# Performance work log

Hardware: AMD Instinct MI355X
Metric: run time of the kernel (lower is better)

The kernel has to match this reference:

```python
import jax, jax.numpy as jnp
import numpy as np

N_NODES = 50000
N_EDGES = 1_600_000
D_IN = 128
D_HID = 128
N_CLASSES = 8
N_GRAPHS = 64


def setup_inputs() -> dict:
    key = jax.random.key(0)
    ks = jax.random.split(key, 8)
    x = jax.random.normal(ks[0], (N_NODES, D_IN), dtype=jnp.float32)
    edge_index = jax.random.randint(ks[1], (2, N_EDGES), 0, N_NODES, dtype=jnp.int32)
    graph_ids = jnp.sort(jax.random.randint(ks[2], (N_NODES,), 0, N_GRAPHS, dtype=jnp.int32))
    s = 1.0 / np.sqrt(D_HID)
    W1 = jax.random.normal(ks[3], (D_IN, D_HID), dtype=jnp.float32) * s
    b1 = jnp.zeros((D_HID,), dtype=jnp.float32)
    W2 = jax.random.normal(ks[4], (D_HID, D_HID), dtype=jnp.float32) * s
    b2 = jnp.zeros((D_HID,), dtype=jnp.float32)
    Wc = jax.random.normal(ks[5], (D_HID, N_CLASSES), dtype=jnp.float32) * s
    bc = jnp.zeros((N_CLASSES,), dtype=jnp.float32)
    return {"x": x, "edge_index": edge_index, "graph_ids": graph_ids,
            "W1": W1, "b1": b1, "W2": W2, "b2": b2, "Wc": Wc, "bc": bc}


def _gcn_layer(h, src, dst, norm, W, b):
    # message: gather source features, apply symmetric degree normalization
    msg = h[src] * norm[:, None]                       # [E, d]
    agg = jax.ops.segment_sum(msg, dst, num_segments=N_NODES)  # [N, d]
    return jax.nn.relu(agg @ W + b)


def reference(x, edge_index, graph_ids, W1, b1, W2, b2, Wc, bc):
    src, dst = edge_index[0], edge_index[1]
    ones_e = jnp.ones((N_EDGES,), dtype=x.dtype)
    deg = jax.ops.segment_sum(ones_e, dst, num_segments=N_NODES)
    deg_inv_sqrt = jnp.where(deg > 0, jax.lax.rsqrt(jnp.maximum(deg, 1.0)), 0.0)
    norm = deg_inv_sqrt[src] * deg_inv_sqrt[dst]       # [E]

    h = _gcn_layer(x, src, dst, norm, W1, b1)
    h = _gcn_layer(h, src, dst, norm, W2, b2)

    # per-graph mean pooling (segment mean over nodes of each graph)
    ones_n = jnp.ones((N_NODES,), dtype=h.dtype)
    counts = jax.ops.segment_sum(ones_n, graph_ids, num_segments=N_GRAPHS)
    pooled = jax.ops.segment_sum(h, graph_ids, num_segments=N_GRAPHS)
    pooled = pooled / jnp.maximum(counts, 1.0)[:, None]  # [G, d]

    logits = pooled @ Wc + bc                           # [G, n_classes]
    return logits
```

## Files before the change

### kernel.cpp

```cpp
#include <hip/hip_runtime.h>
#include <hip/hip_bf16.h>

#define D_HID 128
#define N_GRAPHS 64
#define N_CLASSES 8
#define NPB 16
#define CAP 96
#define KSWEEP 8

__device__ inline unsigned short f2b(float x) {
    unsigned int u = __float_as_uint(x);
    unsigned int r = (u + 0x7fffu + ((u >> 16) & 1u)) >> 16;
    return (unsigned short)r;
}
__device__ inline float b2f(unsigned short u) {
    return __uint_as_float((unsigned int)u << 16);
}

__global__ __launch_bounds__(256) void prep_kernel(const float* __restrict__ x,
                                                   unsigned int* __restrict__ xb,
                                                   int castBlocks, int n2,
                                                   const int* __restrict__ src,
                                                   const int* __restrict__ dst,
                                                   int* __restrict__ cursor,
                                                   unsigned short* __restrict__ csr16,
                                                   int E, int N, int fillBlocks, int rangeSize) {
    const int b = blockIdx.x;
    if (b < castBlocks) {
        int i = b * 256 + threadIdx.x;
        if (i < n2) {
            float a = x[2 * i], c = x[2 * i + 1];
            xb[i] = (unsigned int)f2b(a) | ((unsigned int)f2b(c) << 16);
        }
        return;
    }
    const int fb = b - castBlocks;
    const int sweep = fb / fillBlocks;
    const int blk = fb - sweep * fillBlocks;
    const int e = blk * 256 + threadIdx.x;
    if (e >= E) return;
    const int d = dst[e];
    const int lo = sweep * rangeSize;
    if (d < lo || d >= lo + rangeSize) return;
    const int s = src[e];
    int slot = atomicAdd(&cursor[d], 1);
    if (slot < CAP) csr16[(size_t)slot * N + d] = (unsigned short)s;
}

__global__ __launch_bounds__(256) void dis_counts_kernel(const int* __restrict__ deg,
                                                         float* __restrict__ dis,
                                                         const int* __restrict__ gid,
                                                         int* __restrict__ counts, int N) {
    int n = blockIdx.x * blockDim.x + threadIdx.x;
    if (n < N) {
        int v = deg[n];
        dis[n] = (v > 0) ? rsqrtf((float)v) : 0.0f;
    }
    if (blockIdx.x == 0 && threadIdx.x < N_GRAPHS) {
        int g = threadIdx.x;
        int lo0 = 0, hi0 = N;
        while (lo0 < hi0) { int mid = (lo0 + hi0) >> 1; if (gid[mid] < g) lo0 = mid + 1; else hi0 = mid; }
        int lo1 = lo0, hi1 = N;
        while (lo1 < hi1) { int mid = (lo1 + hi1) >> 1; if (gid[mid] < g + 1) lo1 = mid + 1; else hi1 = mid; }
        counts[g] = lo1 - lo0;
    }
}

__global__ __launch_bounds__(256) void layer_kernel(const unsigned short* __restrict__ h_in,
                                                    const int* __restrict__ deg,
                                                    const unsigned short* __restrict__ csr16,
                                                    const float* __restrict__ dis,
                                                    const float* __restrict__ W,
                                                    const float* __restrict__ bias,
                                                    unsigned short* __restrict__ h_out,
                                                    float* __restrict__ pooled,
                                                    const int* __restrict__ gid,
                                                    int fuse_pool, int N) {
    const int base = blockIdx.x * NPB;
    const int tid = threadIdx.x;
    const int wv = tid >> 6;
    const int lane = tid & 63;
    const int q = lane >> 4;
    const int ql = lane & 15;
    __shared__ float s_agg[NPB][D_HID];

    #pragma unroll
    for (int p = 0; p < 2; ++p) {
        const int n0 = base + wv * 4 + p * 2;
        const int n1 = n0 + 1;
        float acc0[8] = {0.f, 0.f, 0.f, 0.f, 0.f, 0.f, 0.f, 0.f};
        float acc1[8] = {0.f, 0.f, 0.f, 0.f, 0.f, 0.f, 0.f, 0.f};
        const int d0 = (n0 < N) ? min(deg[n0], CAP) : 0;
        const int d1 = (n1 < N) ? min(deg[n1], CAP) : 0;
        const int dm = max(d0, d1);
        for (int cb = 0; cb < dm; cb += 64) {
            const int cm = min(64, dm - cb);
            const int c0 = min(64, max(0, d0 - cb));
            const int c1 = min(64, max(0, d1 - cb));
            int idx0 = 0, idx1 = 0;
            float w0 = 0.0f, w1 = 0.0f;
            if (lane < c0) { idx0 = (int)csr16[(size_t)(cb + lane) * N + n0]; w0 = dis[idx0]; }
            if (lane < c1) { idx1 = (int)csr16[(size_t)(cb + lane) * N + n1]; w1 = dis[idx1]; }
            #pragma unroll 4
            for (int j = 0; j < cm; j += 4) {
                const int e = j + q;
                const int s0 = __shfl(idx0, e);
                const float ww0 = __shfl(w0, e);
                const int s1 = __shfl(idx1, e);
                const float ww1 = __shfl(w1, e);
                const uint4 r0 = *(const uint4*)&h_in[(size_t)s0 * D_HID + ql * 8];
                const uint4 r1 = *(const uint4*)&h_in[(size_t)s1 * D_HID + ql * 8];
                acc0[0] = fmaf(ww0, __uint_as_float(r0.x << 16), acc0[0]);
                acc0[1] = fmaf(ww0, __uint_as_float(r0.x & 0xffff0000u), acc0[1]);
                acc0[2] = fmaf(ww0, __uint_as_float(r0.y << 16), acc0[2]);
                acc0[3] = fmaf(ww0, __uint_as_float(r0.y & 0xffff0000u), acc0[3]);
                acc0[4] = fmaf(ww0, __uint_as_float(r0.z << 16), acc0[4]);
                acc0[5] = fmaf(ww0, __uint_as_float(r0.z & 0xffff0000u), acc0[5]);
                acc0[6] = fmaf(ww0, __uint_as_float(r0.w << 16), acc0[6]);
                acc0[7] = fmaf(ww0, __uint_as_float(r0.w & 0xffff0000u), acc0[7]);
                acc1[0] = fmaf(ww1, __uint_as_float(r1.x << 16), acc1[0]);
                acc1[1] = fmaf(ww1, __uint_as_float(r1.x & 0xffff0000u), acc1[1]);
                acc1[2] = fmaf(ww1, __uint_as_float(r1.y << 16), acc1[2]);
                acc1[3] = fmaf(ww1, __uint_as_float(r1.y & 0xffff0000u), acc1[3]);
                acc1[4] = fmaf(ww1, __uint_as_float(r1.z << 16), acc1[4]);
                acc1[5] = fmaf(ww1, __uint_as_float(r1.z & 0xffff0000u), acc1[5]);
                acc1[6] = fmaf(ww1, __uint_as_float(r1.w << 16), acc1[6]);
                acc1[7] = fmaf(ww1, __uint_as_float(r1.w & 0xffff0000u), acc1[7]);
            }
        }
        #pragma unroll
        for (int k = 0; k < 8; ++k) {
            acc0[k] += __shfl_down(acc0[k], 32);
            acc0[k] += __shfl_down(acc0[k], 16);
            acc1[k] += __shfl_down(acc1[k], 32);
            acc1[k] += __shfl_down(acc1[k], 16);
        }
        if (q == 0) {
            const float dn0 = (n0 < N) ? dis[n0] : 0.0f;
            const float dn1 = (n1 < N) ? dis[n1] : 0.0f;
            #pragma unroll
            for (int k = 0; k < 8; ++k) {
                s_agg[wv * 4 + p * 2 + 0][ql * 8 + k] = acc0[k] * dn0;
                s_agg[wv * 4 + p * 2 + 1][ql * 8 + k] = acc1[k] * dn1;
            }
        }
    }
    __syncthreads();

    const int t = tid & 127;
    const int nb = tid >> 7;
    float outv[8];
    const float bt = bias[t];
    #pragma unroll
    for (int i = 0; i < 8; ++i) outv[i] = bt;

    for (int k = 0; k < D_HID; k += 4) {
        const float w0 = W[(k + 0) * D_HID + t];
        const float w1 = W[(k + 1) * D_HID + t];
        const float w2 = W[(k + 2) * D_HID + t];
        const float w3 = W[(k + 3) * D_HID + t];
        #pragma unroll
        for (int i = 0; i < 8; ++i) {
            float4 a = *(const float4*)&s_agg[nb * 8 + i][k];
            outv[i] = fmaf(a.x, w0, outv[i]);
            outv[i] = fmaf(a.y, w1, outv[i]);
            outv[i] = fmaf(a.z, w2, outv[i]);
            outv[i] = fmaf(a.w, w3, outv[i]);
        }
    }

    #pragma unroll
    for (int i = 0; i < 8; ++i) {
        const int n = base + nb * 8 + i;
        if (n >= N) break;
        float v = fmaxf(outv[i], 0.0f);
        if (fuse_pool) {
            atomicAdd(&pooled[gid[n] * D_HID + t], v);
        } else {
            h_out[(size_t)n * D_HID + t] = f2b(v);
        }
    }
}

__global__ __launch_bounds__(128) void pool_kernel(const unsigned short* __restrict__ h,
                                                   const int* __restrict__ gid,
                                                   float* __restrict__ pooled,
                                                   int N, int nodes_per_block) {
    const int t = threadIdx.x;
    const int start = blockIdx.x * nodes_per_block;
    if (start >= N) return;
    const int endn = min(start + nodes_per_block, N);
    int cur = gid[start];
    float sum = 0.0f;
    for (int n = start; n < endn; ++n) {
        int g = gid[n];
        if (g != cur) {
            atomicAdd(&pooled[cur * D_HID + t], sum);
            cur = g; sum = 0.0f;
        }
        sum += b2f(h[(size_t)n * D_HID + t]);
    }
    atomicAdd(&pooled[cur * D_HID + t], sum);
}

__global__ __launch_bounds__(512) void classify_kernel(const float* __restrict__ pooled,
                                                       const int* __restrict__ counts,
                                                       const float* __restrict__ Wc,
                                                       const float* __restrict__ bc,
                                                       float* __restrict__ out) {
    const int g = threadIdx.x >> 3;
    const int c = threadIdx.x & 7;
    float inv = 1.0f / fmaxf((float)counts[g], 1.0f);
    float acc = bc[c];
    #pragma unroll 8
    for (int k = 0; k < D_HID; ++k) {
        acc = fmaf(pooled[g * D_HID + k] * inv, Wc[k * N_CLASSES + c], acc);
    }
    out[g * N_CLASSES + c] = acc;
}

extern "C" void kernel_launch(void* const* d_in, const int* in_sizes, int n_in,
                              void* d_out, int out_size, void* d_ws, size_t ws_size,
                              hipStream_t stream) {
    const float* x   = (const float*)d_in[0];
    const int* edge  = (const int*)d_in[1];
    const int* gid   = (const int*)d_in[2];
    const float* W1  = (const float*)d_in[3];
    const float* b1  = (const float*)d_in[4];
    const float* W2  = (const float*)d_in[5];
    const float* b2  = (const float*)d_in[6];
    const float* Wc  = (const float*)d_in[7];
    const float* bc  = (const float*)d_in[8];
    float* out       = (float*)d_out;

    const int E = in_sizes[1] / 2;
    const int N = in_sizes[2];
    const int* src = edge;
    const int* dst = edge + E;

    char* p = (char*)d_ws;
    auto take = [&](size_t bytes) {
        char* r = p;
        p += (bytes + 255) & ~(size_t)255;
        return r;
    };
    int*   cursor  = (int*)take((size_t)N * 4);
    float* dis     = (float*)take((size_t)N * 4);
    float* pooled  = (float*)take((size_t)N_GRAPHS * D_HID * 4);
    int*   counts  = (int*)take((size_t)N_GRAPHS * 4);
    unsigned short* csr16 = (unsigned short*)take((size_t)N * CAP * 2);
    unsigned short* xb  = (unsigned short*)take((size_t)N * D_HID * 2);
    unsigned short* h1b = (unsigned short*)take((size_t)N * D_HID * 2);
    size_t used = (size_t)(p - (char*)d_ws);
    size_t h2_bytes = (size_t)N * D_HID * 2;
    const bool separate_pool = (used + h2_bytes <= ws_size);
    unsigned short* h2b = separate_pool ? (unsigned short*)take(h2_bytes) : nullptr;

    hipMemsetAsync(cursor, 0, (size_t)N * 4, stream);
    hipMemsetAsync(pooled, 0, (size_t)N_GRAPHS * D_HID * 4, stream);

    const int EB = 256;
    const int n2 = (N * D_HID) / 2;
    const int castBlocks = (n2 + EB - 1) / EB;
    const int fillBlocks = (E + EB - 1) / EB;
    const int rangeSize = (N + KSWEEP - 1) / KSWEEP;
    prep_kernel<<<castBlocks + KSWEEP * fillBlocks, EB, 0, stream>>>(
        x, (unsigned int*)xb, castBlocks, n2, src, dst, cursor, csr16, E, N, fillBlocks, rangeSize);
    dis_counts_kernel<<<(N + EB - 1) / EB, EB, 0, stream>>>(cursor, dis, gid, counts, N);

    const int LG = (N + NPB - 1) / NPB;
    layer_kernel<<<LG, 256, 0, stream>>>(xb, cursor, csr16, dis, W1, b1, h1b, pooled, gid, 0, N);

    if (separate_pool) {
        layer_kernel<<<LG, 256, 0, stream>>>(h1b, cursor, csr16, dis, W2, b2, h2b, pooled, gid, 0, N);
        const int NPBLK = 32;
        pool_kernel<<<(N + NPBLK - 1) / NPBLK, 128, 0, stream>>>(h2b, gid, pooled, N, NPBLK);
    } else {
        layer_kernel<<<LG, 256, 0, stream>>>(h1b, cursor, csr16, dis, W2, b2, nullptr, pooled, gid, 1, N);
    }

    classify_kernel<<<1, 512, 0, stream>>>(pooled, counts, Wc, bc, out);
}
```

Baseline: 376.3 us.

## Pack bf16 source norm with index in CSR, vectorize cast, always fuse pooling

```diff
diff --git a/kernel.cpp b/kernel.cpp
--- a/kernel.cpp
+++ b/kernel.cpp
@@ -18,19 +18,22 @@
 }
 
 __global__ __launch_bounds__(256) void prep_kernel(const float* __restrict__ x,
-                                                   unsigned int* __restrict__ xb,
-                                                   int castBlocks, int n2,
+                                                   uint2* __restrict__ xb4,
+                                                   int castBlocks, int n4,
                                                    const int* __restrict__ src,
                                                    const int* __restrict__ dst,
                                                    int* __restrict__ cursor,
-                                                   unsigned short* __restrict__ csr16,
+                                                   unsigned int* __restrict__ csr32,
                                                    int E, int N, int fillBlocks, int rangeSize) {
     const int b = blockIdx.x;
     if (b < castBlocks) {
         int i = b * 256 + threadIdx.x;
-        if (i < n2) {
-            float a = x[2 * i], c = x[2 * i + 1];
-            xb[i] = (unsigned int)f2b(a) | ((unsigned int)f2b(c) << 16);
+        if (i < n4) {
+            float4 v = ((const float4*)x)[i];
+            uint2 o;
+            o.x = (unsigned int)f2b(v.x) | ((unsigned int)f2b(v.y) << 16);
+            o.y = (unsigned int)f2b(v.z) | ((unsigned int)f2b(v.w) << 16);
+            xb4[i] = o;
         }
         return;
     }
@@ -44,7 +47,7 @@
     if (d < lo || d >= lo + rangeSize) return;
     const int s = src[e];
     int slot = atomicAdd(&cursor[d], 1);
-    if (slot < CAP) csr16[(size_t)slot * N + d] = (unsigned short)s;
+    if (slot < CAP) csr32[(size_t)slot * N + d] = (unsigned int)s;
 }
 
 __global__ __launch_bounds__(256) void dis_counts_kernel(const int* __restrict__ deg,
@@ -66,16 +69,29 @@
     }
 }
 
-__global__ __launch_bounds__(256) void layer_kernel(const unsigned short* __restrict__ h_in,
-                                                    const int* __restrict__ deg,
-                                                    const unsigned short* __restrict__ csr16,
-                                                    const float* __restrict__ dis,
-                                                    const float* __restrict__ W,
-                                                    const float* __restrict__ bias,
-                                                    unsigned short* __restrict__ h_out,
-                                                    float* __restrict__ pooled,
-                                                    const int* __restrict__ gid,
-                                                    int fuse_pool, int N) {
+__global__ __launch_bounds__(256) void pack_kernel(unsigned int* __restrict__ csr32,
+                                                   const int* __restrict__ deg,
+                                                   const float* __restrict__ dis, int N) {
+    const int n = blockIdx.x * 256 + threadIdx.x;
+    const int slot = blockIdx.y;
+    if (n >= N) return;
+    if (slot < min(deg[n], CAP)) {
+        const size_t i = (size_t)slot * N + n;
+        unsigned int v = csr32[i];
+        csr32[i] = v | ((unsigned int)f2b(dis[v & 0xffffu]) << 16);
+    }
+}
+
+__global__ __launch_bounds__(256, 8) void layer_kernel(const unsigned short* __restrict__ h_in,
+                                                       const int* __restrict__ deg,
+                                                       const unsigned int* __restrict__ csr32,
+                                                       const float* __restrict__ dis,
+                                                       const float* __restrict__ W,
+                                                       const float* __restrict__ bias,
+                                                       unsigned short* __restrict__ h_out,
+                                                       float* __restrict__ pooled,
+                                                       const int* __restrict__ gid,
+                                                       int fuse_pool, int N) {
     const int base = blockIdx.x * NPB;
     const int tid = threadIdx.x;
     const int wv = tid >> 6;
@@ -97,19 +113,18 @@
             const int cm = min(64, dm - cb);
             const int c0 = min(64, max(0, d0 - cb));
             const int c1 = min(64, max(0, d1 - cb));
-            int idx0 = 0, idx1 = 0;
-            float w0 = 0.0f, w1 = 0.0f;
-            if (lane < c0) { idx0 = (int)csr16[(size_t)(cb + lane) * N + n0]; w0 = dis[idx0]; }
-            if (lane < c1) { idx1 = (int)csr16[(size_t)(cb + lane) * N + n1]; w1 = dis[idx1]; }
-            #pragma unroll 4
+            unsigned int pk0 = 0, pk1 = 0;
+            if (lane < c0) pk0 = csr32[(size_t)(cb + lane) * N + n0];
+            if (lane < c1) pk1 = csr32[(size_t)(cb + lane) * N + n1];
+            #pragma unroll 8
             for (int j = 0; j < cm; j += 4) {
                 const int e = j + q;
-                const int s0 = __shfl(idx0, e);
-                const float ww0 = __shfl(w0, e);
-                const int s1 = __shfl(idx1, e);
-                const float ww1 = __shfl(w1, e);
-                const uint4 r0 = *(const uint4*)&h_in[(size_t)s0 * D_HID + ql * 8];
-                const uint4 r1 = *(const uint4*)&h_in[(size_t)s1 * D_HID + ql * 8];
+                const unsigned int p0 = (unsigned int)__shfl((int)pk0, e);
+                const unsigned int p1 = (unsigned int)__shfl((int)pk1, e);
+                const float ww0 = __uint_as_float(p0 & 0xffff0000u);
+                const float ww1 = __uint_as_float(p1 & 0xffff0000u);
+                const uint4 r0 = *(const uint4*)&h_in[(size_t)(p0 & 0xffffu) * D_HID + ql * 8];
+                const uint4 r1 = *(const uint4*)&h_in[(size_t)(p1 & 0xffffu) * D_HID + ql * 8];
                 acc0[0] = fmaf(ww0, __uint_as_float(r0.x << 16), acc0[0]);
                 acc0[1] = fmaf(ww0, __uint_as_float(r0.x & 0xffff0000u), acc0[1]);
                 acc0[2] = fmaf(ww0, __uint_as_float(r0.y << 16), acc0[2]);
@@ -182,27 +197,6 @@
     }
 }
 
-__global__ __launch_bounds__(128) void pool_kernel(const unsigned short* __restrict__ h,
-                                                   const int* __restrict__ gid,
-                                                   float* __restrict__ pooled,
-                                                   int N, int nodes_per_block) {
-    const int t = threadIdx.x;
-    const int start = blockIdx.x * nodes_per_block;
-    if (start >= N) return;
-    const int endn = min(start + nodes_per_block, N);
-    int cur = gid[start];
-    float sum = 0.0f;
-    for (int n = start; n < endn; ++n) {
-        int g = gid[n];
-        if (g != cur) {
-            atomicAdd(&pooled[cur * D_HID + t], sum);
-            cur = g; sum = 0.0f;
-        }
-        sum += b2f(h[(size_t)n * D_HID + t]);
-    }
-    atomicAdd(&pooled[cur * D_HID + t], sum);
-}
-
 __global__ __launch_bounds__(512) void classify_kernel(const float* __restrict__ pooled,
                                                        const int* __restrict__ counts,
                                                        const float* __restrict__ Wc,
@@ -248,36 +242,26 @@
     float* dis     = (float*)take((size_t)N * 4);
     float* pooled  = (float*)take((size_t)N_GRAPHS * D_HID * 4);
     int*   counts  = (int*)take((size_t)N_GRAPHS * 4);
-    unsigned short* csr16 = (unsigned short*)take((size_t)N * CAP * 2);
+    unsigned int* csr32 = (unsigned int*)take((size_t)N * CAP * 4);
     unsigned short* xb  = (unsigned short*)take((size_t)N * D_HID * 2);
     unsigned short* h1b = (unsigned short*)take((size_t)N * D_HID * 2);
-    size_t used = (size_t)(p - (char*)d_ws);
-    size_t h2_bytes = (size_t)N * D_HID * 2;
-    const bool separate_pool = (used + h2_bytes <= ws_size);
-    unsigned short* h2b = separate_pool ? (unsigned short*)take(h2_bytes) : nullptr;
 
     hipMemsetAsync(cursor, 0, (size_t)N * 4, stream);
     hipMemsetAsync(pooled, 0, (size_t)N_GRAPHS * D_HID * 4, stream);
 
     const int EB = 256;
-    const int n2 = (N * D_HID) / 2;
-    const int castBlocks = (n2 + EB - 1) / EB;
+    const int n4 = (N * D_HID) / 4;
+    const int castBlocks = (n4 + EB - 1) / EB;
     const int fillBlocks = (E + EB - 1) / EB;
     const int rangeSize = (N + KSWEEP - 1) / KSWEEP;
     prep_kernel<<<castBlocks + KSWEEP * fillBlocks, EB, 0, stream>>>(
-        x, (unsigned int*)xb, castBlocks, n2, src, dst, cursor, csr16, E, N, fillBlocks, rangeSize);
+        x, (uint2*)xb, castBlocks, n4, src, dst, cursor, csr32, E, N, fillBlocks, rangeSize);
     dis_counts_kernel<<<(N + EB - 1) / EB, EB, 0, stream>>>(cursor, dis, gid, counts, N);
+    pack_kernel<<<dim3((N + EB - 1) / EB, CAP), EB, 0, stream>>>(csr32, cursor, dis, N);
 
     const int LG = (N + NPB - 1) / NPB;
-    layer_kernel<<<LG, 256, 0, stream>>>(xb, cursor, csr16, dis, W1, b1, h1b, pooled, gid, 0, N);
-
-    if (separate_pool) {
-        layer_kernel<<<LG, 256, 0, stream>>>(h1b, cursor, csr16, dis, W2, b2, h2b, pooled, gid, 0, N);
-        const int NPBLK = 32;
-        pool_kernel<<<(N + NPBLK - 1) / NPBLK, 128, 0, stream>>>(h2b, gid, pooled, N, NPBLK);
-    } else {
-        layer_kernel<<<LG, 256, 0, stream>>>(h1b, cursor, csr16, dis, W2, b2, nullptr, pooled, gid, 1, N);
-    }
+    layer_kernel<<<LG, 256, 0, stream>>>(xb, cursor, csr32, dis, W1, b1, h1b, pooled, gid, 0, N);
+    layer_kernel<<<LG, 256, 0, stream>>>(h1b, cursor, csr32, dis, W2, b2, nullptr, pooled, gid, 1, N);
 
     classify_kernel<<<1, 512, 0, stream>>>(pooled, counts, Wc, bc, out);
 }
```

Result: slower. 395.5 us (+5.1%).
